# Kernel optimization log

Hardware: AMD Instinct MI355X
Metric: run time of the kernel (lower is better)

Reference implementation:

```python
import jax, jax.numpy as jnp
import numpy as np

B, N, H = 32, 256, 1024
HEADS, NHID = 8, 128
NCLS = 7
BAND = 24
ALPHA = 0.2          # GAT leaky-relu slope
NEG = -9e15          # masked-attention fill, as in pyGAT


def setup_inputs() -> dict:
    key = jax.random.key(0)
    ks = jax.random.split(key, 16)
    def nrm(k, shp, s=0.02):
        return jax.random.normal(k, shp, dtype=jnp.float32) * s
    hidden_cls = jax.random.normal(ks[0], (B, N, H), dtype=jnp.float32)
    hidden_emo = jax.random.normal(ks[1], (B, N, H), dtype=jnp.float32)
    # causal band cliques, diagonal included (GAT uses clique - eye)
    t = jnp.arange(N)
    band = ((t[None, :] <= t[:, None]) & (t[None, :] > t[:, None] - BAND)).astype(jnp.float32)
    clique = jnp.broadcast_to(band, (B, N, N))
    labels = jax.random.randint(ks[2], (B, N), 0, NCLS)
    pooler_W = nrm(ks[3], (H, H)); pooler_b = jnp.zeros((H,), jnp.float32)
    gat_W = nrm(ks[4], (HEADS, H, NHID))
    gat_a1 = nrm(ks[5], (HEADS, NHID)); gat_a2 = nrm(ks[6], (HEADS, NHID))
    out_W = nrm(ks[7], (H, H))            # heads*nhid == H -> nclass=H
    out_a1 = nrm(ks[8], (H,)); out_a2 = nrm(ks[9], (H,))
    lin1_W = nrm(ks[10], (H, H)); lin1_b = jnp.zeros((H,), jnp.float32)
    lin0_W = nrm(ks[11], (2 * H, H)); lin0_b = jnp.zeros((H,), jnp.float32)
    cls_W = nrm(ks[12], (H, NCLS)); cls_b = jnp.zeros((NCLS,), jnp.float32)
    A = jax.random.uniform(ks[13], (NCLS, NCLS), dtype=jnp.float32) + 0.1
    hmm_A = A / A.sum(axis=1, keepdims=True)   # row-stochastic transition matrix
    return dict(hidden_cls=hidden_cls, hidden_emo=hidden_emo, clique=clique,
                labels=labels, pooler_W=pooler_W, pooler_b=pooler_b,
                gat_W=gat_W, gat_a1=gat_a1, gat_a2=gat_a2,
                out_W=out_W, out_a1=out_a1, out_a2=out_a2,
                lin1_W=lin1_W, lin1_b=lin1_b, lin0_W=lin0_W, lin0_b=lin0_b,
                cls_W=cls_W, cls_b=cls_b, hmm_A=hmm_A)


def _lrelu(x):
    return jnp.where(x > 0, x, ALPHA * x)


def reference(hidden_cls, hidden_emo, clique, labels, pooler_W, pooler_b,
              gat_W, gat_a1, gat_a2, out_W, out_a1, out_a2,
              lin1_W, lin1_b, lin0_W, lin0_b, cls_W, cls_b, hmm_A):
    # PoolerAll: dense + tanh on all token states (dropout = identity in eval)
    fea_cls = jnp.tanh(hidden_cls @ pooler_W + pooler_b)   # [B,N,H] (CLS per utt)
    fea_emo = jnp.tanh(hidden_emo @ pooler_W + pooler_b)   # [B,N,H] (mask tok per utt)

    eyeN = jnp.eye(N, dtype=clique.dtype)
    adjm = (clique - eyeN) > 0                             # [B,N,N] GAT adjacency

    def gat_one(x, am):                                    # x [N,H], am [N,N]
        Wh = jnp.einsum('nf,hfd->hnd', x, gat_W)           # [heads,N,nhid]
        e = _lrelu(jnp.einsum('hnd,hd->hn', Wh, gat_a1)[:, :, None]
                   + jnp.einsum('hnd,hd->hn', Wh, gat_a2)[:, None, :])
        att = jax.nn.softmax(jnp.where(am[None], e, NEG), axis=-1)
        h1 = jax.nn.elu(jnp.einsum('hnm,hmd->hnd', att, Wh))
        h1 = jnp.transpose(h1, (1, 0, 2)).reshape(N, HEADS * NHID)
        Wh2 = h1 @ out_W                                   # out attention layer (concat=False)
        e2 = _lrelu((Wh2 @ out_a1)[:, None] + (Wh2 @ out_a2)[None, :])
        h2 = jax.nn.softmax(jnp.where(am, e2, NEG), axis=-1) @ Wh2
        return jax.nn.elu(h2)                              # [N,H]

    gat_out = jax.vmap(gat_one)(fea_cls, adjm)             # [B,N,H]
    # row 0 replaced by (dropout of) fea_cls row 0, as in the original
    g = jnp.concatenate([fea_cls[:, :1], gat_out[:, 1:]], axis=1)
    g = jnp.concatenate([fea_cls, g @ lin1_W + lin1_b], axis=-1) @ lin0_W + lin0_b
    log_gat = jax.nn.softmax(g @ cls_W + cls_b, axis=-1)   # [B,N,NCLS] (probs)

    # HMM emission probs hmm_B(fea) = softmax(classifier(fea))
    Bprob = jax.nn.softmax(fea_emo @ cls_W + cls_b, axis=-1)  # [B,N,NCLS]
    P0 = jnp.full((NCLS,), 1.0 / NCLS, dtype=jnp.float32)
    AT = hmm_A.T

    def hmm_row(Bp, mrow):                                 # Bp [N,NCLS], mrow [N]
        def step(carry, xs):
            p, started = carry
            bt, m = xs
            p_init = P0 * bt; p_init = p_init / p_init.sum()
            p_tr = (AT @ p) * bt; p_tr = p_tr / p_tr.sum()
            p_new = jnp.where(started, p_tr, p_init)
            valid = m > 0.5
            return (jnp.where(valid, p_new, p), started | valid), None
        (p, _), _ = jax.lax.scan(step, (P0, jnp.asarray(False)), (Bp, mrow))
        return p                                           # final filtered posterior

    log_hmm = jax.vmap(lambda Bp, M: jax.vmap(lambda mr: hmm_row(Bp, mr))(M))(Bprob, clique)

    logits = jnp.log((log_gat + log_hmm) * 0.5).reshape(B * N, NCLS)
    lab = labels.reshape(B * N)
    mask = lab >= 0
    picked = jnp.take_along_axis(logits, jnp.where(mask, lab, 0)[:, None], axis=1)[:, 0]
    loss = -(jnp.where(mask, picked, 0.0).sum() / jnp.maximum(mask.sum(), 1).astype(jnp.float32))
    return loss, logits
```

## Files before the change

### kernel.cpp

```cpp
#include <hip/hip_runtime.h>
#include <hip/hip_bf16.h>
#include <math.h>

typedef __hip_bfloat16 bf16;
typedef __attribute__((ext_vector_type(8))) short short8;
typedef __attribute__((ext_vector_type(4))) float float4v;

static constexpr int Bb = 32, Nn = 256, Hh = 1024, HEADS = 8, NHID = 128, NCLS = 7, BAND = 24;
static constexpr int M = Bb * Nn;
static constexpr float ALPHA = 0.2f;
static constexpr long INEL = (long)M * Hh;

__device__ __forceinline__ float tof(bf16 x) { return __bfloat162float(x); }
__device__ __forceinline__ bf16 tob(float x) { return __float2bfloat16(x); }
__device__ __forceinline__ unsigned short f2bits(float x) {
    bf16 h = __float2bfloat16(x);
    return *(unsigned short*)&h;
}
__device__ __forceinline__ float bits2f(unsigned short u) {
    unsigned v = ((unsigned)u) << 16;
    float f;
    __builtin_memcpy(&f, &v, 4);
    return f;
}

__device__ __forceinline__ void gload16(const void* g, void* l) {
    __builtin_amdgcn_global_load_lds(
        (const __attribute__((address_space(1))) void*)g,
        (__attribute__((address_space(3))) void*)l, 16, 0, 0);
}

static constexpr long OFF_PWT  = 0;
static constexpr long OFF_PB   = 1048576;
static constexpr long OFF_WCT  = 1049600;
static constexpr long OFF_GA1  = 2098176;
static constexpr long OFF_GA2  = 2099200;
static constexpr long OFF_OWT  = 2100224;
static constexpr long OFF_OA1  = 3148800;
static constexpr long OFF_OA2  = 3149824;
static constexpr long OFF_L1WT = 3150848;
static constexpr long OFF_L1B  = 4199424;
static constexpr long OFF_L0WT = 4200448;
static constexpr long OFF_L0B  = 6297600;
static constexpr long OFF_CWT  = 6298624;
static constexpr long OFF_CB   = 6305792;
static constexpr long OFF_HA   = 6305799;
static constexpr long W_TOTAL  = 6305848;

__global__ void probe_k(const void* __restrict__ p, int* __restrict__ flag) {
    int t = threadIdx.x;
    int bad = 0;
    for (int i = t; i < 4096; i += 256) {
        float v = tof(((const bf16*)p)[i]);
        if (!(fabsf(v) < 1e4f)) bad = 1;
    }
    __shared__ int sb[256];
    sb[t] = bad; __syncthreads();
    for (int s = 128; s; s >>= 1) { if (t < s) sb[t] |= sb[t + s]; __syncthreads(); }
    if (t == 0) *flag = sb[0] ? 0 : 1;
}

__device__ __forceinline__ float ldany(const void* p, long i, int isb) {
    return isb ? tof(((const bf16*)p)[i]) : ((const float*)p)[i];
}

__global__ void convert_k(const int* __restrict__ flagp,
                          const void* pW, const void* pb, const void* gW,
                          const void* ga1, const void* ga2, const void* oW,
                          const void* oa1, const void* oa2, const void* l1W,
                          const void* l1b, const void* l0W, const void* l0b,
                          const void* cW, const void* cb, const void* hA,
                          bf16* __restrict__ dst) {
    long idx = (long)blockIdx.x * 256 + threadIdx.x;
    if (idx >= W_TOTAL) return;
    if ((idx >= OFF_L1WT && idx < OFF_L1B) || (idx >= OFF_L0WT && idx < OFF_L0B)) return;
    int isb = *flagp;
    const void* src; long si;
    if      (idx < OFF_PB)   { long l = idx;            long n = l >> 10, k = l & 1023;
                               src = pW;  si = k * 1024 + n; }
    else if (idx < OFF_WCT)  { src = pb;  si = idx - OFF_PB; }
    else if (idx < OFF_GA1)  { long l = idx - OFF_WCT;  long n = l >> 10, f = l & 1023;
                               long h = n >> 7, d = n & 127;
                               src = gW;  si = h * 131072 + f * 128 + d; }
    else if (idx < OFF_GA2)  { src = ga1; si = idx - OFF_GA1; }
    else if (idx < OFF_OWT)  { src = ga2; si = idx - OFF_GA2; }
    else if (idx < OFF_OA1)  { long l = idx - OFF_OWT;  long n = l >> 10, k = l & 1023;
                               src = oW;  si = k * 1024 + n; }
    else if (idx < OFF_OA2)  { src = oa1; si = idx - OFF_OA1; }
    else if (idx < OFF_L1WT) { src = oa2; si = idx - OFF_OA2; }
    else if (idx < OFF_L0WT) { src = l1b; si = idx - OFF_L1B; }
    else if (idx < OFF_CWT)  { src = l0b; si = idx - OFF_L0B; }
    else if (idx < OFF_CB)   { long l = idx - OFF_CWT;  long c = l >> 10, k = l & 1023;
                               src = cW;  si = k * 7 + c; }
    else if (idx < OFF_HA)   { src = cb;  si = idx - OFF_CB; }
    else                     { src = hA;  si = idx - OFF_HA; }
    dst[idx] = tob(ldany(src, si, isb));
}

__global__ void convin_k(const int* __restrict__ flagp, const void* __restrict__ s0,
                         const void* __restrict__ s1, bf16* __restrict__ d0,
                         bf16* __restrict__ d1) {
    const int isb = *flagp;
    if (isb) return;
    long i = ((long)blockIdx.x * 256 + threadIdx.x) * 8;
    const void* s; bf16* d; long off;
    if (i < INEL) { s = s0; d = d0; off = i; }
    else          { s = s1; d = d1; off = i - INEL; }
    const float* f = (const float*)s + off;
    unsigned short tmp[8];
    #pragma unroll
    for (int q = 0; q < 8; ++q) tmp[q] = f2bits(f[q]);
    *(int4*)(d + off) = *(int4*)tmp;
}

__global__ void gvec_k(const int* __restrict__ flagp, const void* __restrict__ l0W,
                       const void* __restrict__ cWr, float* __restrict__ W1T,
                       float* __restrict__ Gb) {
    int k = blockIdx.x;
    int lane = threadIdx.x;
    int isb = *flagp;
    float acc[NCLS];
    #pragma unroll
    for (int c = 0; c < NCLS; ++c) acc[c] = 0.f;
    #pragma unroll
    for (int q = 0; q < 16; ++q) {
        int j = lane * 16 + q;
        float x = ldany(l0W, (long)k * 1024 + j, isb);
        #pragma unroll
        for (int c = 0; c < NCLS; ++c) acc[c] += x * ldany(cWr, (long)j * 7 + c, isb);
    }
    #pragma unroll
    for (int c = 0; c < NCLS; ++c)
        #pragma unroll
        for (int off = 32; off; off >>= 1) acc[c] += __shfl_down(acc[c], off);
    if (lane == 0) {
        #pragma unroll
        for (int c = 0; c < NCLS; ++c) {
            if (k < 1024) W1T[c * 1024 + k] = acc[c];
            else          Gb[(k - 1024) * 7 + c] = acc[c];
        }
    }
}

__global__ void w2_k(const int* __restrict__ flagp, const void* __restrict__ l1W,
                     const float* __restrict__ Gb, float* __restrict__ W2T) {
    int i = blockIdx.x;
    int lane = threadIdx.x;
    int isb = *flagp;
    float acc[NCLS];
    #pragma unroll
    for (int c = 0; c < NCLS; ++c) acc[c] = 0.f;
    #pragma unroll
    for (int q = 0; q < 16; ++q) {
        int o = lane * 16 + q;
        float x = ldany(l1W, (long)i * 1024 + o, isb);
        #pragma unroll
        for (int c = 0; c < NCLS; ++c) acc[c] += x * Gb[o * 7 + c];
    }
    #pragma unroll
    for (int c = 0; c < NCLS; ++c)
        #pragma unroll
        for (int off = 32; off; off >>= 1) acc[c] += __shfl_down(acc[c], off);
    if (lane == 0) {
        #pragma unroll
        for (int c = 0; c < NCLS; ++c) W2T[c * 1024 + i] = acc[c];
    }
}

__global__ void cvec_k(const int* __restrict__ flagp, const void* __restrict__ l1b,
                       const void* __restrict__ l0b, const void* __restrict__ cWr,
                       const void* __restrict__ cbr, const float* __restrict__ Gb,
                       float* __restrict__ cvec) {
    int lane = threadIdx.x;
    int isb = *flagp;
    float acc[NCLS];
    #pragma unroll
    for (int c = 0; c < NCLS; ++c) acc[c] = 0.f;
    for (int o = lane; o < 1024; o += 64) {
        float b1 = ldany(l1b, o, isb);
        float b0 = ldany(l0b, o, isb);
        #pragma unroll
        for (int c = 0; c < NCLS; ++c)
            acc[c] += b1 * Gb[o * 7 + c] + b0 * ldany(cWr, (long)o * 7 + c, isb);
    }
    #pragma unroll
    for (int c = 0; c < NCLS; ++c)
        #pragma unroll
        for (int off = 32; off; off >>= 1) acc[c] += __shfl_down(acc[c], off);
    if (lane == 0) {
        #pragma unroll
        for (int c = 0; c < NCLS; ++c) cvec[c] = acc[c] + ldany(cbr, c, isb);
    }
}

static constexpr int SLOT_US = 256 * 32;

template <int ACT>
__device__ __forceinline__ void gemm_pipe_core(
    const bf16* __restrict__ A0, const bf16* __restrict__ A1, int ksw,
    int strideA, const bf16* __restrict__ Bt, int strideB,
    const bf16* __restrict__ bias, bf16* __restrict__ Cout,
    int Nc, int K, int bm, int bn, unsigned short* lds) {
    const int tid = threadIdx.x;
    const int lane = tid & 63;
    const int wave = tid >> 6;
    const int wm = (wave >> 1) * 64, wn = (wave & 1) * 64;
    const int l15 = lane & 15, quad = lane >> 4;
    const int csw = ((lane & 3) ^ ((lane >> 2) & 3) ^ (lane >> 4)) * 8;
    const int sc8 = (quad ^ (l15 & 3) ^ (l15 >> 2)) * 8;

    long aoff[2], boff[2];
    #pragma unroll
    for (int o = 0; o < 2; ++o) {
        aoff[o] = (long)(bm + wave * 32 + o * 16 + (lane >> 2)) * strideA + csw;
        boff[o] = (long)(bn + wave * 32 + o * 16 + (lane >> 2)) * strideB + csw;
    }
    const int aDst = wave * 32 * 32;
    const int bDst = (128 + wave * 32) * 32;

    const int nt = K / 32;
    float4v acc[4][4];
    #pragma unroll
    for (int i = 0; i < 4; ++i)
        #pragma unroll
        for (int j = 0; j < 4; ++j) acc[i][j] = (float4v){0.f, 0.f, 0.f, 0.f};

    auto stage = [&](int ts, int slot) {
        unsigned short* buf = lds + slot * SLOT_US;
        int ksub = ts * 32;
        const bf16* Ap = A0; int ka = ksub;
        if (ksub >= ksw) { Ap = A1; ka = ksub - ksw; }
        gload16(Ap + aoff[0] + ka, buf + aDst);
        gload16(Ap + aoff[1] + ka, buf + aDst + 512);
        gload16(Bt + boff[0] + ksub, buf + bDst);
        gload16(Bt + boff[1] + ksub, buf + bDst + 512);
    };
    auto frags = [&](int slot, short8* af, short8* bfr) {
        const unsigned short* bufc = lds + slot * SLOT_US;
        #pragma unroll
        for (int i = 0; i < 4; ++i)
            af[i] = *(const short8*)(bufc + (wm + i * 16 + l15) * 32 + sc8);
        #pragma unroll
        for (int j = 0; j < 4; ++j)
            bfr[j] = *(const short8*)(bufc + (128 + wn + j * 16 + l15) * 32 + sc8);
    };

    stage(0, 0); stage(1, 1); stage(2, 2);
    asm volatile("s_waitcnt vmcnt(8)" ::: "memory");
    __builtin_amdgcn_s_barrier();
    asm volatile("" ::: "memory");
    short8 afA[4], bfA[4], afB[4], bfB[4];
    frags(0, afA, bfA);
    int c0 = 0, c1 = 1, c2 = 2;

    for (int t = 0; t < nt; t += 2) {
        asm volatile("s_waitcnt lgkmcnt(0)" ::: "memory");
        if (t < nt - 2) asm volatile("s_waitcnt vmcnt(4)" ::: "memory");
        else            asm volatile("s_waitcnt vmcnt(0)" ::: "memory");
        __builtin_amdgcn_s_barrier();
        asm volatile("" ::: "memory");
        if (t + 3 < nt) stage(t + 3, c0);
        if (t + 1 < nt) frags(c1, afB, bfB);
        __builtin_amdgcn_s_setprio(1);
        #pragma unroll
        for (int i = 0; i < 4; ++i)
            #pragma unroll
            for (int j = 0; j < 4; ++j)
                acc[i][j] = __builtin_amdgcn_mfma_f32_16x16x32_bf16(afA[i], bfA[j], acc[i][j], 0, 0, 0);
        __builtin_amdgcn_s_setprio(0);
        asm volatile("" ::: "memory");
        asm volatile("s_waitcnt lgkmcnt(0)" ::: "memory");
        if (t + 1 < nt - 2) asm volatile("s_waitcnt vmcnt(4)" ::: "memory");
        else                asm volatile("s_waitcnt vmcnt(0)" ::: "memory");
        __builtin_amdgcn_s_barrier();
        asm volatile("" ::: "memory");
        if (t + 4 < nt) stage(t + 4, c1);
        if (t + 2 < nt) frags(c2, afA, bfA);
        __builtin_amdgcn_s_setprio(1);
        #pragma unroll
        for (int i = 0; i < 4; ++i)
            #pragma unroll
            for (int j = 0; j < 4; ++j)
                acc[i][j] = __builtin_amdgcn_mfma_f32_16x16x32_bf16(afB[i], bfB[j], acc[i][j], 0, 0, 0);
        __builtin_amdgcn_s_setprio(0);
        asm volatile("" ::: "memory");
        int n0 = c2, n1 = c0, n2 = c1;
        c0 = n0; c1 = n1; c2 = n2;
    }

    #pragma unroll
    for (int j = 0; j < 4; ++j) {
        int gn = bn + wn + j * 16 + l15;
        float bj = bias ? tof(bias[gn]) : 0.f;
        #pragma unroll
        for (int i = 0; i < 4; ++i) {
            #pragma unroll
            for (int r = 0; r < 4; ++r) {
                int gm = bm + wm + i * 16 + quad * 4 + r;
                float v = acc[i][j][r] + bj;
                if (ACT == 1) v = tanhf(v);
                Cout[(long)gm * Nc + gn] = tob(v);
            }
        }
    }
}

template <int ACT>
__global__ __launch_bounds__(256, 3) void gemm_pipe_k(const bf16* __restrict__ A,
                                                      const bf16* __restrict__ Bt,
                                                      const bf16* __restrict__ bias,
                                                      bf16* __restrict__ Cout,
                                                      int Nc, int K) {
    __shared__ __align__(16) unsigned short lds[3 * SLOT_US];
    gemm_pipe_core<ACT>(A, A, K, K, Bt, K, bias, Cout, Nc, K,
                        blockIdx.x * 128, blockIdx.y * 128, lds);
}

__global__ __launch_bounds__(256, 3) void gemmP_pipe_k(const int* __restrict__ flagp,
                                                       const bf16* __restrict__ rawE,
                                                       const bf16* __restrict__ rawC,
                                                       const bf16* __restrict__ A0,
                                                       const bf16* __restrict__ A1,
                                                       const bf16* __restrict__ Bt,
                                                       const bf16* __restrict__ bias,
                                                       bf16* __restrict__ C0,
                                                       bf16* __restrict__ C1) {
    __shared__ __align__(16) unsigned short lds[3 * SLOT_US];
    const int isb = *flagp;
    const bf16* A = blockIdx.z ? (isb ? rawC : A1) : (isb ? rawE : A0);
    bf16* C = blockIdx.z ? C1 : C0;
    gemm_pipe_core<1>(A, A, Hh, Hh, Bt, Hh, bias, C, Hh, Hh,
                      blockIdx.x * 128, blockIdx.y * 128, lds);
}

__global__ __launch_bounds__(256) void att1f_k(const bf16* __restrict__ Wh,
                                               const bf16* __restrict__ ga1,
                                               const bf16* __restrict__ ga2,
                                               bf16* __restrict__ h1) {
    __shared__ unsigned short S[152][128];
    __shared__ float f1s[152], f2s[152];
    __shared__ float att[128][25];
    const int bx = blockIdx.x;
    const int b = bx >> 4, h = (bx >> 1) & 7, half = bx & 1;
    const int nbase = half * 128;
    const int mstart = half ? (nbase - (BAND - 1)) : 0;
    const int mcount = half ? (256 - mstart) : 128;
    const int t = threadIdx.x;
    const int c = t & 15;

    float av1[8], av2[8];
    {
        union { int4 v; unsigned short us[8]; } u1, u2;
        u1.v = *(const int4*)(ga1 + h * 128 + c * 8);
        u2.v = *(const int4*)(ga2 + h * 128 + c * 8);
        #pragma unroll
        for (int qq = 0; qq < 8; ++qq) { av1[qq] = bits2f(u1.us[qq]); av2[qq] = bits2f(u2.us[qq]); }
    }

    const int iters = (mcount * 16 + 255) >> 8;
    for (int i = 0; i < iters; ++i) {
        int li = i * 256 + t;
        int mr = li >> 4;
        if (mr < mcount) {
            long ga = (long)(b * 256 + mstart + mr) * 1024 + h * 128 + c * 8;
            union { int4 v; unsigned short us[8]; } u;
            u.v = *(const int4*)(Wh + ga);
            float p1 = 0.f, p2 = 0.f;
            #pragma unroll
            for (int qq = 0; qq < 8; ++qq) {
                float f = bits2f(u.us[qq]);
                p1 += f * av1[qq]; p2 += f * av2[qq];
            }
            *(int4*)&S[mr][c * 8] = u.v;
            #pragma unroll
            for (int mask = 1; mask < 16; mask <<= 1) {
                p1 += __shfl_xor(p1, mask);
                p2 += __shfl_xor(p2, mask);
            }
            if (c == 0) { f1s[mr] = p1; f2s[mr] = p2; }
        }
    }
    __syncthreads();

    if (t < 128) {
        int n = nbase + t;
        if (n > 0) {
            int cnt = n < (BAND - 1) ? n : (BAND - 1);
            int m0 = n - cnt;
            float f1n = f1s[n - mstart];
            float e[BAND - 1];
            float mx = -1e30f;
            for (int i = 0; i < cnt; ++i) {
                float v = f1n + f2s[m0 + i - mstart];
                v = v > 0.f ? v : ALPHA * v;
                e[i] = v; mx = fmaxf(mx, v);
            }
            float ss = 0.f;
            for (int i = 0; i < cnt; ++i) { e[i] = __expf(e[i] - mx); ss += e[i]; }
            float inv = 1.0f / ss;
            for (int i = 0; i < cnt; ++i) att[t][i] = e[i] * inv;
        }
    }
    __syncthreads();

    const int wave = t >> 6, lane = t & 63;
    for (int ln = wave; ln < 128; ln += 4) {
        int n = nbase + ln;
        if (n == 0) continue;
        int cnt = n < (BAND - 1) ? n : (BAND - 1);
        int mr0 = n - cnt - mstart;
        float s0 = 0.f, s1 = 0.f;
        for (int i = 0; i < cnt; ++i) {
            float a = att[ln][i];
            unsigned u = *(const unsigned*)&S[mr0 + i][lane * 2];
            s0 += a * bits2f((unsigned short)(u & 0xffff));
            s1 += a * bits2f((unsigned short)(u >> 16));
        }
        s0 = s0 > 0.f ? s0 : expm1f(s0);
        s1 = s1 > 0.f ? s1 : expm1f(s1);
        unsigned out = (unsigned)f2bits(s0) | ((unsigned)f2bits(s1) << 16);
        *(unsigned*)(h1 + (long)(b * 256 + n) * 1024 + h * 128 + lane * 2) = out;
    }
}

__global__ void mean1_k(const bf16* __restrict__ Wh, bf16* __restrict__ h1) {
    int bh = blockIdx.x;
    int h = bh & 7, b = bh >> 3;
    int lane = threadIdx.x;
    float s0 = 0.f, s1 = 0.f;
    long base = (long)(b * 256) * 1024 + h * 128 + lane * 2;
    for (int m = 0; m < 256; ++m) {
        unsigned u = *(const unsigned*)(Wh + base + (long)m * 1024);
        s0 += bits2f((unsigned short)(u & 0xffff));
        s1 += bits2f((unsigned short)(u >> 16));
    }
    s0 *= (1.0f / 256.0f); s1 *= (1.0f / 256.0f);
    s0 = s0 > 0.f ? s0 : expm1f(s0);
    s1 = s1 > 0.f ? s1 : expm1f(s1);
    unsigned out = (unsigned)f2bits(s0) | ((unsigned)f2bits(s1) << 16);
    *(unsigned*)(h1 + base) = out;
}

__global__ void f12b_k(const bf16* __restrict__ Wh2, const bf16* __restrict__ a1,
                       const bf16* __restrict__ a2, float* __restrict__ f1b,
                       float* __restrict__ f2b) {
    int idx = blockIdx.x;
    int lane = threadIdx.x;
    const bf16* row = Wh2 + (long)idx * 1024 + lane * 16;
    float s1 = 0.f, s2 = 0.f;
    #pragma unroll
    for (int half = 0; half < 2; ++half) {
        union { int4 v; unsigned short us[8]; } x, w1, w2;
        x.v  = *(const int4*)(row + half * 8);
        w1.v = *(const int4*)(a1 + lane * 16 + half * 8);
        w2.v = *(const int4*)(a2 + lane * 16 + half * 8);
        #pragma unroll
        for (int q = 0; q < 8; ++q) {
            float f = bits2f(x.us[q]);
            s1 += f * bits2f(w1.us[q]);
            s2 += f * bits2f(w2.us[q]);
        }
    }
    #pragma unroll
    for (int off = 32; off; off >>= 1) {
        s1 += __shfl_down(s1, off);
        s2 += __shfl_down(s2, off);
    }
    if (lane == 0) { f1b[idx] = s1; f2b[idx] = s2; }
}

__global__ __launch_bounds__(256) void att2f_k(const bf16* __restrict__ Wh2,
                                               const float* __restrict__ f1b,
                                               const float* __restrict__ f2b,
                                               bf16* __restrict__ g) {
    __shared__ unsigned short S[152][128];
    __shared__ float att[128][25];
    const int bx = blockIdx.x;
    const int b = bx >> 4, half = (bx >> 3) & 1, jt = bx & 7;
    const int nbase = half * 128;
    const int mstart = half ? (nbase - (BAND - 1)) : 0;
    const int mcount = half ? (256 - mstart) : 128;
    const int t = threadIdx.x;
    const int c = t & 15;

    const int iters = (mcount * 16 + 255) >> 8;
    for (int i = 0; i < iters; ++i) {
        int li = i * 256 + t;
        int mr = li >> 4;
        if (mr < mcount) {
            long ga = (long)(b * 256 + mstart + mr) * 1024 + jt * 128 + c * 8;
            *(int4*)&S[mr][c * 8] = *(const int4*)(Wh2 + ga);
        }
    }
    __syncthreads();

    if (t < 128) {
        int n = nbase + t;
        if (n > 0) {
            int cnt = n < (BAND - 1) ? n : (BAND - 1);
            int m0 = n - cnt;
            float f1n = f1b[b * 256 + n];
            float e[BAND - 1];
            float mx = -1e30f;
            for (int i = 0; i < cnt; ++i) {
                float v = f1n + f2b[b * 256 + m0 + i];
                v = v > 0.f ? v : ALPHA * v;
                e[i] = v; mx = fmaxf(mx, v);
            }
            float ss = 0.f;
            for (int i = 0; i < cnt; ++i) { e[i] = __expf(e[i] - mx); ss += e[i]; }
            float inv = 1.0f / ss;
            for (int i = 0; i < cnt; ++i) att[t][i] = e[i] * inv;
        }
    }
    __syncthreads();

    const int wave = t >> 6, lane = t & 63;
    for (int ln = wave; ln < 128; ln += 4) {
        int n = nbase + ln;
        if (n == 0) continue;
        int cnt = n < (BAND - 1) ? n : (BAND - 1);
        int mr0 = n - cnt - mstart;
        float s0 = 0.f, s1 = 0.f;
        for (int i = 0; i < cnt; ++i) {
            float a = att[ln][i];
            unsigned u = *(const unsigned*)&S[mr0 + i][lane * 2];
            s0 += a * bits2f((unsigned short)(u & 0xffff));
            s1 += a * bits2f((unsigned short)(u >> 16));
        }
        s0 = s0 > 0.f ? s0 : expm1f(s0);
        s1 = s1 > 0.f ? s1 : expm1f(s1);
        unsigned out = (unsigned)f2bits(s0) | ((unsigned)f2bits(s1) << 16);
        *(unsigned*)(g + (long)(b * 256 + n) * 1024 + jt * 128 + lane * 2) = out;
    }
}

__global__ void g_row0_k(const bf16* __restrict__ fea_cls, bf16* __restrict__ g) {
    int b = blockIdx.x;
    int t = threadIdx.x;
    long base = (long)(b * 256) * 1024 + t * 8;
    *(int4*)(g + base) = *(const int4*)(fea_cls + base);
}

__global__ void cls7_k(const bf16* __restrict__ X, const bf16* __restrict__ Wt,
                       const bf16* __restrict__ b, float* __restrict__ out, int K) {
    int row = blockIdx.x;
    int lane = threadIdx.x;
    float xv[16];
    {
        const bf16* x = X + (long)row * K + lane * 16;
        union { int4 v; unsigned short us[8]; } u0, u1;
        u0.v = *(const int4*)x; u1.v = *(const int4*)(x + 8);
        #pragma unroll
        for (int q = 0; q < 8; ++q) { xv[q] = bits2f(u0.us[q]); xv[q + 8] = bits2f(u1.us[q]); }
    }
    float acc[NCLS];
    #pragma unroll
    for (int cc = 0; cc < NCLS; ++cc) {
        const bf16* wr = Wt + (long)cc * K + lane * 16;
        union { int4 v; unsigned short us[8]; } w0, w1;
        w0.v = *(const int4*)wr; w1.v = *(const int4*)(wr + 8);
        float s = 0.f;
        #pragma unroll
        for (int q = 0; q < 8; ++q) {
            s += xv[q] * bits2f(w0.us[q]);
            s += xv[q + 8] * bits2f(w1.us[q]);
        }
        acc[cc] = s;
    }
    #pragma unroll
    for (int cc = 0; cc < NCLS; ++cc)
        #pragma unroll
        for (int off = 32; off; off >>= 1) acc[cc] += __shfl_down(acc[cc], off);
    if (lane == 0) {
        float mx = -1e30f;
        #pragma unroll
        for (int cc = 0; cc < NCLS; ++cc) { acc[cc] += tof(b[cc]); mx = fmaxf(mx, acc[cc]); }
        float s = 0.f;
        #pragma unroll
        for (int cc = 0; cc < NCLS; ++cc) { acc[cc] = expf(acc[cc] - mx); s += acc[cc]; }
        float inv = 1.0f / s;
        #pragma unroll
        for (int cc = 0; cc < NCLS; ++cc) out[(long)row * NCLS + cc] = acc[cc] * inv;
    }
}

__global__ void lgat2_k(const bf16* __restrict__ X, const bf16* __restrict__ Y,
                        const float* __restrict__ W1T, const float* __restrict__ W2T,
                        const float* __restrict__ cvec, float* __restrict__ out) {
    int row = blockIdx.x;
    int lane = threadIdx.x;
    float xv[16], yv[16];
    {
        const bf16* x = X + (long)row * 1024 + lane * 16;
        const bf16* y = Y + (long)row * 1024 + lane * 16;
        union { int4 v; unsigned short us[8]; } u0, u1, v0, v1;
        u0.v = *(const int4*)x; u1.v = *(const int4*)(x + 8);
        v0.v = *(const int4*)y; v1.v = *(const int4*)(y + 8);
        #pragma unroll
        for (int q = 0; q < 8; ++q) {
            xv[q] = bits2f(u0.us[q]); xv[q + 8] = bits2f(u1.us[q]);
            yv[q] = bits2f(v0.us[q]); yv[q + 8] = bits2f(v1.us[q]);
        }
    }
    float acc[NCLS];
    #pragma unroll
    for (int cc = 0; cc < NCLS; ++cc) {
        const float4* w1 = (const float4*)(W1T + (long)cc * 1024 + lane * 16);
        const float4* w2 = (const float4*)(W2T + (long)cc * 1024 + lane * 16);
        float s = 0.f;
        #pragma unroll
        for (int h = 0; h < 4; ++h) {
            float4 a = w1[h], b = w2[h];
            s += xv[h * 4 + 0] * a.x + xv[h * 4 + 1] * a.y + xv[h * 4 + 2] * a.z + xv[h * 4 + 3] * a.w;
            s += yv[h * 4 + 0] * b.x + yv[h * 4 + 1] * b.y + yv[h * 4 + 2] * b.z + yv[h * 4 + 3] * b.w;
        }
        acc[cc] = s;
    }
    #pragma unroll
    for (int cc = 0; cc < NCLS; ++cc)
        #pragma unroll
        for (int off = 32; off; off >>= 1) acc[cc] += __shfl_down(acc[cc], off);
    if (lane == 0) {
        float mx = -1e30f;
        #pragma unroll
        for (int cc = 0; cc < NCLS; ++cc) { acc[cc] += cvec[cc]; mx = fmaxf(mx, acc[cc]); }
        float s = 0.f;
        #pragma unroll
        for (int cc = 0; cc < NCLS; ++cc) { acc[cc] = expf(acc[cc] - mx); s += acc[cc]; }
        float inv = 1.0f / s;
        #pragma unroll
        for (int cc = 0; cc < NCLS; ++cc) out[(long)row * NCLS + cc] = acc[cc] * inv;
    }
}

__global__ void hmm_k(const float* __restrict__ Bprob, const bf16* __restrict__ hmm_A,
                      float* __restrict__ out) {
    __shared__ float AT[NCLS][NCLS];
    int t = threadIdx.x;
    if (t < NCLS * NCLS) {
        int i = t / NCLS, j = t % NCLS;
        AT[i][j] = tof(hmm_A[j * NCLS + i]);
    }
    __syncthreads();
    int idx = blockIdx.x * blockDim.x + t;
    int n = idx & 255, b = idx >> 8;
    int t0 = n - (BAND - 1) > 0 ? n - (BAND - 1) : 0;
    const float* Bp = Bprob + (long)(b * 256) * NCLS;
    float p[NCLS];
    float s = 0.f;
    #pragma unroll
    for (int cc = 0; cc < NCLS; ++cc) { p[cc] = Bp[t0 * NCLS + cc]; s += p[cc]; }
    float inv = 1.0f / s;
    #pragma unroll
    for (int cc = 0; cc < NCLS; ++cc) p[cc] *= inv;
    for (int tt = t0 + 1; tt <= n; ++tt) {
        float q[NCLS]; float ss = 0.f;
        #pragma unroll
        for (int i = 0; i < NCLS; ++i) {
            float a = 0.f;
            #pragma unroll
            for (int j = 0; j < NCLS; ++j) a += AT[i][j] * p[j];
            a *= Bp[tt * NCLS + i];
            q[i] = a; ss += a;
        }
        float iv = 1.0f / ss;
        #pragma unroll
        for (int i = 0; i < NCLS; ++i) p[i] = q[i] * iv;
    }
    #pragma unroll
    for (int cc = 0; cc < NCLS; ++cc) out[(long)idx * NCLS + cc] = p[cc];
}

__global__ void zero_k(float* p) { *p = 0.f; }

__global__ void final_k(const float* __restrict__ lg, const float* __restrict__ lh,
                        const int* __restrict__ labels, void* __restrict__ out,
                        float* __restrict__ loss_acc, const int* __restrict__ flagp) {
    int idx = blockIdx.x * blockDim.x + threadIdx.x;
    const int isb = *flagp;
    float lo[NCLS];
    int lab = labels[idx];
    #pragma unroll
    for (int c = 0; c < NCLS; ++c) {
        float v = logf(0.5f * (lg[(long)idx * NCLS + c] + lh[(long)idx * NCLS + c]));
        lo[c] = v;
        long o = 1 + (long)idx * NCLS + c;
        if (isb) ((bf16*)out)[o] = tob(v);
        else     ((float*)out)[o] = v;
    }
    float picked = lo[lab];
    __shared__ float red[256];
    red[threadIdx.x] = picked;
    __syncthreads();
    for (int s = 128; s; s >>= 1) {
        if (threadIdx.x < s) red[threadIdx.x] += red[threadIdx.x + s];
        __syncthreads();
    }
    if (threadIdx.x == 0) atomicAdd(loss_acc, red[0]);
}

__global__ void loss_k(const float* __restrict__ acc, void* __restrict__ out,
                       const int* __restrict__ flagp) {
    float v = -acc[0] / (float)(Bb * Nn);
    if (*flagp) ((bf16*)out)[0] = tob(v);
    else        ((float*)out)[0] = v;
}

extern "C" void kernel_launch(void* const* d_in, const int* in_sizes, int n_in,
                              void* d_out, int out_size, void* d_ws, size_t ws_size,
                              hipStream_t stream) {
    const void* hidden_cls = d_in[0];
    const void* hidden_emo = d_in[1];
    const int* labels = (const int*)d_in[3];

    char* w = (char*)d_ws;
    bf16* C  = (bf16*)w;
    bf16* E  = C + INEL;
    bf16* Wb = E + INEL;
    bf16* H2 = Wb + INEL;
    bf16* wc = H2 + INEL;
    float* f1b   = (float*)(wc + W_TOTAL);
    float* f2b   = f1b + M;
    float* Bprob = f2b + M;
    float* lgat  = Bprob + (long)M * NCLS;
    float* lhmm  = lgat + (long)M * NCLS;
    float* loss_acc = lhmm + (long)M * NCLS;
    int*   flag  = (int*)(loss_acc + 1);
    float* W1f   = (float*)(flag + 1);
    float* W2f   = W1f + 7 * 1024;
    float* Gbf   = W2f + 7 * 1024;
    float* cvec  = Gbf + 1024 * 7;

    dim3 gblk(256);
    dim3 ggrid(M / 128, Hh / 128);
    dim3 pgrid(M / 128, Hh / 128, 2);

    probe_k<<<1, 256, 0, stream>>>(d_in[4], flag);
    convert_k<<<(int)((W_TOTAL + 255) / 256), 256, 0, stream>>>(
        flag, d_in[4], d_in[5], d_in[6], d_in[7], d_in[8], d_in[9], d_in[10],
        d_in[11], d_in[12], d_in[13], d_in[14], d_in[15], d_in[16], d_in[17],
        d_in[18], wc);
    gvec_k<<<2048, 64, 0, stream>>>(flag, d_in[14], d_in[16], W1f, Gbf);
    w2_k<<<1024, 64, 0, stream>>>(flag, d_in[12], Gbf, W2f);
    cvec_k<<<1, 64, 0, stream>>>(flag, d_in[13], d_in[15], d_in[16], d_in[17], Gbf, cvec);
    convin_k<<<(int)(2 * INEL / (256 * 8)), 256, 0, stream>>>(flag, hidden_emo, hidden_cls, Wb, H2);

    gemmP_pipe_k<<<pgrid, gblk, 0, stream>>>(flag, (const bf16*)hidden_emo,
                                             (const bf16*)hidden_cls, Wb, H2,
                                             wc + OFF_PWT, wc + OFF_PB, E, C);
    cls7_k<<<M, 64, 0, stream>>>(E, wc + OFF_CWT, wc + OFF_CB, Bprob, Hh);
    gemm_pipe_k<0><<<ggrid, gblk, 0, stream>>>(C, wc + OFF_WCT, (const bf16*)nullptr, Wb, Hh, Hh);
    att1f_k<<<512, 256, 0, stream>>>(Wb, wc + OFF_GA1, wc + OFF_GA2, E);
    mean1_k<<<Bb * HEADS, 64, 0, stream>>>(Wb, E);
    gemm_pipe_k<0><<<ggrid, gblk, 0, stream>>>(E, wc + OFF_OWT, (const bf16*)nullptr, Wb, Hh, Hh);
    f12b_k<<<M, 64, 0, stream>>>(Wb, wc + OFF_OA1, wc + OFF_OA2, f1b, f2b);
    g_row0_k<<<Bb, 128, 0, stream>>>(C, E);
    att2f_k<<<512, 256, 0, stream>>>(Wb, f1b, f2b, E);
    lgat2_k<<<M, 64, 0, stream>>>(C, E, W1f, W2f, cvec, lgat);
    hmm_k<<<M / 256, 256, 0, stream>>>(Bprob, wc + OFF_HA, lhmm);
    zero_k<<<1, 1, 0, stream>>>(loss_acc);
    final_k<<<M / 256, 256, 0, stream>>>(lgat, lhmm, labels, d_out, loss_acc, flag);
    loss_k<<<1, 1, 0, stream>>>(loss_acc, d_out, flag);
}
```

Baseline: 483.2 us.

## Consolidate prep kernels, tile weight transposes, fold small launches into neighbors

Replaces the per-element weight conversion with a single small-parameter kernel that also computes the dtype flag, plus a shared-memory tiled transpose for the large weight matrices so loads and stores stay coalesced. The gvec and w2 reductions now stage the small 7-column matrix in LDS and process several rows per block. The mean1, g_row0 and zero kernels are folded into att1f, lgat2 and hmm to cut launch count, and hmm runs with smaller blocks for more parallelism. The paired pooler GEMM is split into two launches, which drops the A0/A1 switch inside the GEMM core.

```diff
diff --git a/kernel.cpp b/kernel.cpp
--- a/kernel.cpp
+++ b/kernel.cpp
@@ -38,63 +38,86 @@
 static constexpr long OFF_OWT  = 2100224;
 static constexpr long OFF_OA1  = 3148800;
 static constexpr long OFF_OA2  = 3149824;
-static constexpr long OFF_L1WT = 3150848;
-static constexpr long OFF_L1B  = 4199424;
-static constexpr long OFF_L0WT = 4200448;
-static constexpr long OFF_L0B  = 6297600;
 static constexpr long OFF_CWT  = 6298624;
 static constexpr long OFF_CB   = 6305792;
 static constexpr long OFF_HA   = 6305799;
 static constexpr long W_TOTAL  = 6305848;
 
-__global__ void probe_k(const void* __restrict__ p, int* __restrict__ flag) {
-    int t = threadIdx.x;
+__device__ __forceinline__ float ldany(const void* p, long i, int isb) {
+    return isb ? tof(((const bf16*)p)[i]) : ((const float*)p)[i];
+}
+
+__global__ __launch_bounds__(256) void small_convert_k(
+    const void* pW, const void* pb, const void* ga1, const void* ga2,
+    const void* oa1, const void* oa2, const void* cW, const void* cb,
+    const void* hA, bf16* __restrict__ dst, int* __restrict__ flag) {
+    __shared__ int sb[256];
+    const int t = threadIdx.x;
     int bad = 0;
     for (int i = t; i < 4096; i += 256) {
-        float v = tof(((const bf16*)p)[i]);
+        float v = tof(((const bf16*)pW)[i]);
         if (!(fabsf(v) < 1e4f)) bad = 1;
     }
-    __shared__ int sb[256];
     sb[t] = bad; __syncthreads();
     for (int s = 128; s; s >>= 1) { if (t < s) sb[t] |= sb[t + s]; __syncthreads(); }
-    if (t == 0) *flag = sb[0] ? 0 : 1;
-}
-
-__device__ __forceinline__ float ldany(const void* p, long i, int isb) {
-    return isb ? tof(((const bf16*)p)[i]) : ((const float*)p)[i];
-}
-
-__global__ void convert_k(const int* __restrict__ flagp,
-                          const void* pW, const void* pb, const void* gW,
-                          const void* ga1, const void* ga2, const void* oW,
-                          const void* oa1, const void* oa2, const void* l1W,
-                          const void* l1b, const void* l0W, const void* l0b,
-                          const void* cW, const void* cb, const void* hA,
-                          bf16* __restrict__ dst) {
-    long idx = (long)blockIdx.x * 256 + threadIdx.x;
-    if (idx >= W_TOTAL) return;
-    if ((idx >= OFF_L1WT && idx < OFF_L1B) || (idx >= OFF_L0WT && idx < OFF_L0B)) return;
-    int isb = *flagp;
-    const void* src; long si;
-    if      (idx < OFF_PB)   { long l = idx;            long n = l >> 10, k = l & 1023;
-                               src = pW;  si = k * 1024 + n; }
-    else if (idx < OFF_WCT)  { src = pb;  si = idx - OFF_PB; }
-    else if (idx < OFF_GA1)  { long l = idx - OFF_WCT;  long n = l >> 10, f = l & 1023;
-                               long h = n >> 7, d = n & 127;
-                               src = gW;  si = h * 131072 + f * 128 + d; }
-    else if (idx < OFF_GA2)  { src = ga1; si = idx - OFF_GA1; }
-    else if (idx < OFF_OWT)  { src = ga2; si = idx - OFF_GA2; }
-    else if (idx < OFF_OA1)  { long l = idx - OFF_OWT;  long n = l >> 10, k = l & 1023;
-                               src = oW;  si = k * 1024 + n; }
-    else if (idx < OFF_OA2)  { src = oa1; si = idx - OFF_OA1; }
-    else if (idx < OFF_L1WT) { src = oa2; si = idx - OFF_OA2; }
-    else if (idx < OFF_L0WT) { src = l1b; si = idx - OFF_L1B; }
-    else if (idx < OFF_CWT)  { src = l0b; si = idx - OFF_L0B; }
-    else if (idx < OFF_CB)   { long l = idx - OFF_CWT;  long c = l >> 10, k = l & 1023;
-                               src = cW;  si = k * 7 + c; }
-    else if (idx < OFF_HA)   { src = cb;  si = idx - OFF_CB; }
-    else                     { src = hA;  si = idx - OFF_HA; }
-    dst[idx] = tob(ldany(src, si, isb));
+    const int isb = sb[0] ? 0 : 1;
+    if (t == 0) *flag = isb;
+    for (int i = t; i < 1024; i += 256) {
+        dst[OFF_PB  + i] = tob(ldany(pb,  i, isb));
+        dst[OFF_GA1 + i] = tob(ldany(ga1, i, isb));
+        dst[OFF_GA2 + i] = tob(ldany(ga2, i, isb));
+        dst[OFF_OA1 + i] = tob(ldany(oa1, i, isb));
+        dst[OFF_OA2 + i] = tob(ldany(oa2, i, isb));
+    }
+    for (int i = t; i < 7168; i += 256) {
+        int c = i >> 10, k = i & 1023;
+        dst[OFF_CWT + i] = tob(ldany(cW, (long)k * 7 + c, isb));
+    }
+    if (t < NCLS) dst[OFF_CB + t] = tob(ldany(cb, t, isb));
+    if (t < NCLS * NCLS) dst[OFF_HA + t] = tob(ldany(hA, t, isb));
+}
+
+__global__ __launch_bounds__(256) void transposeT_k(const int* __restrict__ flagp,
+                                                    const void* __restrict__ pW,
+                                                    const void* __restrict__ oW,
+                                                    const void* __restrict__ gW,
+                                                    bf16* __restrict__ dst) {
+    __shared__ float S[64][65];
+    const int isb = *flagp;
+    const int z = blockIdx.z;
+    const int tx = threadIdx.x, ty0 = threadIdx.y;
+    if (z < 2) {
+        const void* src = z ? oW : pW;
+        const long doff = z ? OFF_OWT : OFF_PWT;
+        const int r0 = blockIdx.y * 64, c0 = blockIdx.x * 64;
+        #pragma unroll 4
+        for (int it = 0; it < 16; ++it) {
+            int ty = it * 4 + ty0;
+            S[ty][tx] = ldany(src, (long)(r0 + ty) * 1024 + c0 + tx, isb);
+        }
+        __syncthreads();
+        #pragma unroll 4
+        for (int it = 0; it < 16; ++it) {
+            int ty = it * 4 + ty0;
+            dst[doff + (long)(c0 + ty) * 1024 + r0 + tx] = tob(S[tx][ty]);
+        }
+    } else {
+        if (blockIdx.x >= 2) return;
+        const int h = z - 2;
+        const int r0 = blockIdx.y * 64, c0 = blockIdx.x * 64;
+        const long sbase = (long)h * 131072;
+        #pragma unroll 4
+        for (int it = 0; it < 16; ++it) {
+            int ty = it * 4 + ty0;
+            S[ty][tx] = ldany(gW, sbase + (long)(r0 + ty) * 128 + c0 + tx, isb);
+        }
+        __syncthreads();
+        #pragma unroll 4
+        for (int it = 0; it < 16; ++it) {
+            int ty = it * 4 + ty0;
+            dst[OFF_WCT + (long)(h * 128 + c0 + ty) * 1024 + r0 + tx] = tob(S[tx][ty]);
+        }
+    }
 }
 
 __global__ void convin_k(const int* __restrict__ flagp, const void* __restrict__ s0,
@@ -113,57 +136,81 @@
     *(int4*)(d + off) = *(int4*)tmp;
 }
 
-__global__ void gvec_k(const int* __restrict__ flagp, const void* __restrict__ l0W,
-                       const void* __restrict__ cWr, float* __restrict__ W1T,
-                       float* __restrict__ Gb) {
-    int k = blockIdx.x;
-    int lane = threadIdx.x;
-    int isb = *flagp;
-    float acc[NCLS];
-    #pragma unroll
-    for (int c = 0; c < NCLS; ++c) acc[c] = 0.f;
-    #pragma unroll
-    for (int q = 0; q < 16; ++q) {
-        int j = lane * 16 + q;
-        float x = ldany(l0W, (long)k * 1024 + j, isb);
-        #pragma unroll
-        for (int c = 0; c < NCLS; ++c) acc[c] += x * ldany(cWr, (long)j * 7 + c, isb);
-    }
-    #pragma unroll
-    for (int c = 0; c < NCLS; ++c)
-        #pragma unroll
-        for (int off = 32; off; off >>= 1) acc[c] += __shfl_down(acc[c], off);
-    if (lane == 0) {
-        #pragma unroll
-        for (int c = 0; c < NCLS; ++c) {
-            if (k < 1024) W1T[c * 1024 + k] = acc[c];
-            else          Gb[(k - 1024) * 7 + c] = acc[c];
-        }
-    }
-}
-
-__global__ void w2_k(const int* __restrict__ flagp, const void* __restrict__ l1W,
-                     const float* __restrict__ Gb, float* __restrict__ W2T) {
-    int i = blockIdx.x;
-    int lane = threadIdx.x;
-    int isb = *flagp;
-    float acc[NCLS];
-    #pragma unroll
-    for (int c = 0; c < NCLS; ++c) acc[c] = 0.f;
-    #pragma unroll
-    for (int q = 0; q < 16; ++q) {
-        int o = lane * 16 + q;
-        float x = ldany(l1W, (long)i * 1024 + o, isb);
-        #pragma unroll
-        for (int c = 0; c < NCLS; ++c) acc[c] += x * Gb[o * 7 + c];
-    }
-    #pragma unroll
-    for (int c = 0; c < NCLS; ++c)
-        #pragma unroll
-        for (int off = 32; off; off >>= 1) acc[c] += __shfl_down(acc[c], off);
-    if (lane == 0) {
-        #pragma unroll
-        for (int c = 0; c < NCLS; ++c) W2T[c * 1024 + i] = acc[c];
+__global__ __launch_bounds__(256) void gvec_k(const int* __restrict__ flagp,
+                                              const void* __restrict__ l0W,
+                                              const void* __restrict__ cWr,
+                                              float* __restrict__ W1T,
+                                              float* __restrict__ Gb) {
+    __shared__ float S[1024][NCLS];
+    const int t = threadIdx.x;
+    const int isb = *flagp;
+    for (int j = t; j < 1024; j += 256) {
+        #pragma unroll
+        for (int c = 0; c < NCLS; ++c) S[j][c] = ldany(cWr, (long)j * 7 + c, isb);
+    }
+    __syncthreads();
+    const int wave = t >> 6, lane = t & 63;
+    #pragma unroll
+    for (int r = 0; r < 2; ++r) {
+        int k = blockIdx.x * 8 + wave * 2 + r;
+        float acc[NCLS];
+        #pragma unroll
+        for (int c = 0; c < NCLS; ++c) acc[c] = 0.f;
+        #pragma unroll
+        for (int q = 0; q < 16; ++q) {
+            int j = lane * 16 + q;
+            float x = ldany(l0W, (long)k * 1024 + j, isb);
+            #pragma unroll
+            for (int c = 0; c < NCLS; ++c) acc[c] += x * S[j][c];
+        }
+        #pragma unroll
+        for (int c = 0; c < NCLS; ++c)
+            #pragma unroll
+            for (int off = 32; off; off >>= 1) acc[c] += __shfl_down(acc[c], off);
+        if (lane == 0) {
+            #pragma unroll
+            for (int c = 0; c < NCLS; ++c) {
+                if (k < 1024) W1T[c * 1024 + k] = acc[c];
+                else          Gb[(k - 1024) * 7 + c] = acc[c];
+            }
+        }
+    }
+}
+
+__global__ __launch_bounds__(256) void w2_k(const int* __restrict__ flagp,
+                                            const void* __restrict__ l1W,
+                                            const float* __restrict__ Gb,
+                                            float* __restrict__ W2T) {
+    __shared__ float S[1024][NCLS];
+    const int t = threadIdx.x;
+    const int isb = *flagp;
+    for (int j = t; j < 1024; j += 256) {
+        #pragma unroll
+        for (int c = 0; c < NCLS; ++c) S[j][c] = Gb[(long)j * 7 + c];
+    }
+    __syncthreads();
+    const int wave = t >> 6, lane = t & 63;
+    #pragma unroll
+    for (int r = 0; r < 2; ++r) {
+        int i = blockIdx.x * 8 + wave * 2 + r;
+        float acc[NCLS];
+        #pragma unroll
+        for (int c = 0; c < NCLS; ++c) acc[c] = 0.f;
+        #pragma unroll
+        for (int q = 0; q < 16; ++q) {
+            int o = lane * 16 + q;
+            float x = ldany(l1W, (long)i * 1024 + o, isb);
+            #pragma unroll
+            for (int c = 0; c < NCLS; ++c) acc[c] += x * S[o][c];
+        }
+        #pragma unroll
+        for (int c = 0; c < NCLS; ++c)
+            #pragma unroll
+            for (int off = 32; off; off >>= 1) acc[c] += __shfl_down(acc[c], off);
+        if (lane == 0) {
+            #pragma unroll
+            for (int c = 0; c < NCLS; ++c) W2T[c * 1024 + i] = acc[c];
+        }
     }
 }
 
@@ -197,8 +244,8 @@
 
 template <int ACT>
 __device__ __forceinline__ void gemm_pipe_core(
-    const bf16* __restrict__ A0, const bf16* __restrict__ A1, int ksw,
-    int strideA, const bf16* __restrict__ Bt, int strideB,
+    const bf16* __restrict__ A, int strideA,
+    const bf16* __restrict__ Bt, int strideB,
     const bf16* __restrict__ bias, bf16* __restrict__ Cout,
     int Nc, int K, int bm, int bn, unsigned short* lds) {
     const int tid = threadIdx.x;
@@ -227,13 +274,11 @@
 
     auto stage = [&](int ts, int slot) {
         unsigned short* buf = lds + slot * SLOT_US;
-        int ksub = ts * 32;
-        const bf16* Ap = A0; int ka = ksub;
-        if (ksub >= ksw) { Ap = A1; ka = ksub - ksw; }
-        gload16(Ap + aoff[0] + ka, buf + aDst);
-        gload16(Ap + aoff[1] + ka, buf + aDst + 512);
-        gload16(Bt + boff[0] + ksub, buf + bDst);
-        gload16(Bt + boff[1] + ksub, buf + bDst + 512);
+        int k = ts * 32;
+        gload16(A + aoff[0] + k, buf + aDst);
+        gload16(A + aoff[1] + k, buf + aDst + 512);
+        gload16(Bt + boff[0] + k, buf + bDst);
+        gload16(Bt + boff[1] + k, buf + bDst + 512);
     };
     auto frags = [&](int slot, short8* af, short8* bfr) {
         const unsigned short* bufc = lds + slot * SLOT_US;
@@ -312,24 +357,19 @@
                                                       bf16* __restrict__ Cout,
                                                       int Nc, int K) {
     __shared__ __align__(16) unsigned short lds[3 * SLOT_US];
-    gemm_pipe_core<ACT>(A, A, K, K, Bt, K, bias, Cout, Nc, K,
+    gemm_pipe_core<ACT>(A, K, Bt, K, bias, Cout, Nc, K,
                         blockIdx.x * 128, blockIdx.y * 128, lds);
 }
 
 __global__ __launch_bounds__(256, 3) void gemmP_pipe_k(const int* __restrict__ flagp,
-                                                       const bf16* __restrict__ rawE,
-                                                       const bf16* __restrict__ rawC,
-                                                       const bf16* __restrict__ A0,
-                                                       const bf16* __restrict__ A1,
+                                                       const bf16* __restrict__ rawA,
+                                                       const bf16* __restrict__ convA,
                                                        const bf16* __restrict__ Bt,
                                                        const bf16* __restrict__ bias,
-                                                       bf16* __restrict__ C0,
-                                                       bf16* __restrict__ C1) {
+                                                       bf16* __restrict__ Cout) {
     __shared__ __align__(16) unsigned short lds[3 * SLOT_US];
-    const int isb = *flagp;
-    const bf16* A = blockIdx.z ? (isb ? rawC : A1) : (isb ? rawE : A0);
-    bf16* C = blockIdx.z ? C1 : C0;
-    gemm_pipe_core<1>(A, A, Hh, Hh, Bt, Hh, bias, C, Hh, Hh,
+    const bf16* A = (*flagp) ? rawA : convA;
+    gemm_pipe_core<1>(A, Hh, Bt, Hh, bias, Cout, Hh, Hh,
                       blockIdx.x * 128, blockIdx.y * 128, lds);
 }
 
@@ -337,15 +377,35 @@
                                                const bf16* __restrict__ ga1,
                                                const bf16* __restrict__ ga2,
                                                bf16* __restrict__ h1) {
+    const int bx = blockIdx.x;
+    const int t = threadIdx.x;
+    if (bx >= 512) {
+        if (t < 64) {
+            int bh = bx - 512;
+            int h = bh & 7, b = bh >> 3;
+            int lane = t;
+            float s0 = 0.f, s1 = 0.f;
+            long base = (long)(b * 256) * 1024 + h * 128 + lane * 2;
+            for (int m = 0; m < 256; ++m) {
+                unsigned u = *(const unsigned*)(Wh + base + (long)m * 1024);
+                s0 += bits2f((unsigned short)(u & 0xffff));
+                s1 += bits2f((unsigned short)(u >> 16));
+            }
+            s0 *= (1.0f / 256.0f); s1 *= (1.0f / 256.0f);
+            s0 = s0 > 0.f ? s0 : expm1f(s0);
+            s1 = s1 > 0.f ? s1 : expm1f(s1);
+            unsigned out = (unsigned)f2bits(s0) | ((unsigned)f2bits(s1) << 16);
+            *(unsigned*)(h1 + base) = out;
+        }
+        return;
+    }
     __shared__ unsigned short S[152][128];
     __shared__ float f1s[152], f2s[152];
     __shared__ float att[128][25];
-    const int bx = blockIdx.x;
     const int b = bx >> 4, h = (bx >> 1) & 7, half = bx & 1;
     const int nbase = half * 128;
     const int mstart = half ? (nbase - (BAND - 1)) : 0;
     const int mcount = half ? (256 - mstart) : 128;
-    const int t = threadIdx.x;
     const int c = t & 15;
 
     float av1[8], av2[8];
@@ -423,24 +483,6 @@
     }
 }
 
-__global__ void mean1_k(const bf16* __restrict__ Wh, bf16* __restrict__ h1) {
-    int bh = blockIdx.x;
-    int h = bh & 7, b = bh >> 3;
-    int lane = threadIdx.x;
-    float s0 = 0.f, s1 = 0.f;
-    long base = (long)(b * 256) * 1024 + h * 128 + lane * 2;
-    for (int m = 0; m < 256; ++m) {
-        unsigned u = *(const unsigned*)(Wh + base + (long)m * 1024);
-        s0 += bits2f((unsigned short)(u & 0xffff));
-        s1 += bits2f((unsigned short)(u >> 16));
-    }
-    s0 *= (1.0f / 256.0f); s1 *= (1.0f / 256.0f);
-    s0 = s0 > 0.f ? s0 : expm1f(s0);
-    s1 = s1 > 0.f ? s1 : expm1f(s1);
-    unsigned out = (unsigned)f2bits(s0) | ((unsigned)f2bits(s1) << 16);
-    *(unsigned*)(h1 + base) = out;
-}
-
 __global__ void f12b_k(const bf16* __restrict__ Wh2, const bf16* __restrict__ a1,
                        const bf16* __restrict__ a2, float* __restrict__ f1b,
                        float* __restrict__ f2b) {
@@ -535,13 +577,6 @@
     }
 }
 
-__global__ void g_row0_k(const bf16* __restrict__ fea_cls, bf16* __restrict__ g) {
-    int b = blockIdx.x;
-    int t = threadIdx.x;
-    long base = (long)(b * 256) * 1024 + t * 8;
-    *(int4*)(g + base) = *(const int4*)(fea_cls + base);
-}
-
 __global__ void cls7_k(const bf16* __restrict__ X, const bf16* __restrict__ Wt,
                        const bf16* __restrict__ b, float* __restrict__ out, int K) {
     int row = blockIdx.x;
@@ -590,10 +625,11 @@
                         const float* __restrict__ cvec, float* __restrict__ out) {
     int row = blockIdx.x;
     int lane = threadIdx.x;
+    const bf16* ybase = (row & 255) ? Y : X;
     float xv[16], yv[16];
     {
         const bf16* x = X + (long)row * 1024 + lane * 16;
-        const bf16* y = Y + (long)row * 1024 + lane * 16;
+        const bf16* y = ybase + (long)row * 1024 + lane * 16;
         union { int4 v; unsigned short us[8]; } u0, u1, v0, v1;
         u0.v = *(const int4*)x; u1.v = *(const int4*)(x + 8);
         v0.v = *(const int4*)y; v1.v = *(const int4*)(y + 8);
@@ -635,15 +671,16 @@
 }
 
 __global__ void hmm_k(const float* __restrict__ Bprob, const bf16* __restrict__ hmm_A,
-                      float* __restrict__ out) {
+                      float* __restrict__ out, float* __restrict__ loss_acc) {
     __shared__ float AT[NCLS][NCLS];
     int t = threadIdx.x;
+    if (blockIdx.x == 0 && t == 0) *loss_acc = 0.f;
     if (t < NCLS * NCLS) {
         int i = t / NCLS, j = t % NCLS;
         AT[i][j] = tof(hmm_A[j * NCLS + i]);
     }
     __syncthreads();
-    int idx = blockIdx.x * blockDim.x + t;
+    int idx = blockIdx.x * 64 + t;
     int n = idx & 255, b = idx >> 8;
     int t0 = n - (BAND - 1) > 0 ? n - (BAND - 1) : 0;
     const float* Bp = Bprob + (long)(b * 256) * NCLS;
@@ -671,8 +708,6 @@
     #pragma unroll
     for (int cc = 0; cc < NCLS; ++cc) out[(long)idx * NCLS + cc] = p[cc];
 }
-
-__global__ void zero_k(float* p) { *p = 0.f; }
 
 __global__ void final_k(const float* __restrict__ lg, const float* __restrict__ lh,
                         const int* __restrict__ labels, void* __restrict__ out,
@@ -734,32 +769,29 @@
 
     dim3 gblk(256);
     dim3 ggrid(M / 128, Hh / 128);
-    dim3 pgrid(M / 128, Hh / 128, 2);
-
-    probe_k<<<1, 256, 0, stream>>>(d_in[4], flag);
-    convert_k<<<(int)((W_TOTAL + 255) / 256), 256, 0, stream>>>(
-        flag, d_in[4], d_in[5], d_in[6], d_in[7], d_in[8], d_in[9], d_in[10],
-        d_in[11], d_in[12], d_in[13], d_in[14], d_in[15], d_in[16], d_in[17],
-        d_in[18], wc);
-    gvec_k<<<2048, 64, 0, stream>>>(flag, d_in[14], d_in[16], W1f, Gbf);
-    w2_k<<<1024, 64, 0, stream>>>(flag, d_in[12], Gbf, W2f);
+
+    small_convert_k<<<1, 256, 0, stream>>>(d_in[4], d_in[5], d_in[7], d_in[8],
+                                           d_in[10], d_in[11], d_in[16], d_in[17],
+                                           d_in[18], wc, flag);
+    transposeT_k<<<dim3(16, 16, 10), dim3(64, 4), 0, stream>>>(flag, d_in[4], d_in[9],
+                                                               d_in[6], wc);
+    gvec_k<<<256, 256, 0, stream>>>(flag, d_in[14], d_in[16], W1f, Gbf);
+    w2_k<<<128, 256, 0, stream>>>(flag, d_in[12], Gbf, W2f);
     cvec_k<<<1, 64, 0, stream>>>(flag, d_in[13], d_in[15], d_in[16], d_in[17], Gbf, cvec);
     convin_k<<<(int)(2 * INEL / (256 * 8)), 256, 0, stream>>>(flag, hidden_emo, hidden_cls, Wb, H2);
 
-    gemmP_pipe_k<<<pgrid, gblk, 0, stream>>>(flag, (const bf16*)hidden_emo,
-                                             (const bf16*)hidden_cls, Wb, H2,
-                                             wc + OFF_PWT, wc + OFF_PB, E, C);
+    gemmP_pipe_k<<<ggrid, gblk, 0, stream>>>(flag, (const bf16*)hidden_emo, Wb,
+                                             wc + OFF_PWT, wc + OFF_PB, E);
+    gemmP_pipe_k<<<ggrid, gblk, 0, stream>>>(flag, (const bf16*)hidden_cls, H2,
+                                             wc + OFF_PWT, wc + OFF_PB, C);
     cls7_k<<<M, 64, 0, stream>>>(E, wc + OFF_CWT, wc + OFF_CB, Bprob, Hh);
     gemm_pipe_k<0><<<ggrid, gblk, 0, stream>>>(C, wc + OFF_WCT, (const bf16*)nullptr, Wb, Hh, Hh);
-    att1f_k<<<512, 256, 0, stream>>>(Wb, wc + OFF_GA1, wc + OFF_GA2, E);
-    mean1_k<<<Bb * HEADS, 64, 0, stream>>>(Wb, E);
+    att1f_k<<<768, 256, 0, stream>>>(Wb, wc + OFF_GA1, wc + OFF_GA2, E);
     gemm_pipe_k<0><<<ggrid, gblk, 0, stream>>>(E, wc + OFF_OWT, (const bf16*)nullptr, Wb, Hh, Hh);
     f12b_k<<<M, 64, 0, stream>>>(Wb, wc + OFF_OA1, wc + OFF_OA2, f1b, f2b);
-    g_row0_k<<<Bb, 128, 0, stream>>>(C, E);
     att2f_k<<<512, 256, 0, stream>>>(Wb, f1b, f2b, E);
     lgat2_k<<<M, 64, 0, stream>>>(C, E, W1f, W2f, cvec, lgat);
-    hmm_k<<<M / 256, 256, 0, stream>>>(Bprob, wc + OFF_HA, lhmm);
-    zero_k<<<1, 1, 0, stream>>>(loss_acc);
+    hmm_k<<<M / 64, 64, 0, stream>>>(Bprob, wc + OFF_HA, lhmm, loss_acc);
     final_k<<<M / 256, 256, 0, stream>>>(lgat, lhmm, labels, d_out, loss_acc, flag);
     loss_k<<<1, 1, 0, stream>>>(loss_acc, d_out, flag);
 }
```

Measured after the change: 472.1 us. 1.02x faster.
